# Kernel optimization log

Measured on AMD Instinct MI355X. Metric: run time of the kernel, lower is better.

The kernel has to match this reference:

```python
import jax, jax.numpy as jnp
import numpy as np

B, C, H, W = 4, 256, 48, 48
NH = 4                 # num_heads
HD = C // NH           # head_dim = 64
KD = HD // 2           # key_dim = 32 (attn_ratio=0.5)
QKV_C = C + 2 * KD * NH  # 512
FF = 2 * C             # 512
EPS = 1e-3             # ultralytics BatchNorm2d eps


def _bn(x, g, b, m, v):
    # eval-mode BatchNorm2d over channel dim 1 of NCHW
    s = g / jnp.sqrt(v + EPS)
    return x * s[:, None, None] + (b - m * s)[:, None, None]


def _conv1x1(x, w):
    # w: [out_c, in_c]
    return jnp.einsum('bchw,oc->bohw', x, w)


def _dwconv3x3(x, w):
    # depthwise 3x3, padding 1; w: [C, 1, 3, 3]
    return jax.lax.conv_general_dilated(
        x, w, (1, 1), [(1, 1), (1, 1)],
        dimension_numbers=('NCHW', 'OIHW', 'NCHW'),
        feature_group_count=C)


def setup_inputs() -> dict:
    key = jax.random.key(0)
    ks = jax.random.split(key, 32)
    d = {}
    d['x'] = jax.random.normal(ks[0], (B, C, H, W), dtype=jnp.float32)

    def bn_params(i, ch):
        g = 0.5 + jax.random.uniform(ks[i], (ch,), dtype=jnp.float32)
        b = 0.1 * jax.random.normal(ks[i + 1], (ch,), dtype=jnp.float32)
        m = 0.1 * jax.random.normal(ks[i + 2], (ch,), dtype=jnp.float32)
        v = 0.5 + jax.random.uniform(ks[i + 3], (ch,), dtype=jnp.float32)
        return g, b, m, v

    d['qkv_w'] = 0.05 * jax.random.normal(ks[1], (QKV_C, C), dtype=jnp.float32)
    d['qkv_g'], d['qkv_b'], d['qkv_m'], d['qkv_v'] = bn_params(2, QKV_C)
    d['pe_w'] = 0.1 * jax.random.normal(ks[6], (C, 1, 3, 3), dtype=jnp.float32)
    d['pe_g'], d['pe_b'], d['pe_m'], d['pe_v'] = bn_params(7, C)
    d['proj_w'] = 0.05 * jax.random.normal(ks[11], (C, C), dtype=jnp.float32)
    d['proj_g'], d['proj_b'], d['proj_m'], d['proj_v'] = bn_params(12, C)
    d['f1_w'] = 0.05 * jax.random.normal(ks[16], (FF, C), dtype=jnp.float32)
    d['f1_g'], d['f1_b'], d['f1_m'], d['f1_v'] = bn_params(17, FF)
    d['f2_w'] = 0.05 * jax.random.normal(ks[21], (C, FF), dtype=jnp.float32)
    d['f2_g'], d['f2_b'], d['f2_m'], d['f2_v'] = bn_params(22, C)
    return d


def reference(x, qkv_w, qkv_g, qkv_b, qkv_m, qkv_v,
              pe_w, pe_g, pe_b, pe_m, pe_v,
              proj_w, proj_g, proj_b, proj_m, proj_v,
              f1_w, f1_g, f1_b, f1_m, f1_v,
              f2_w, f2_g, f2_b, f2_m, f2_v):
    b, c, h, w = x.shape
    n = h * w
    # --- Attention ---
    qkv = _bn(_conv1x1(x, qkv_w), qkv_g, qkv_b, qkv_m, qkv_v)
    qkv = qkv.reshape(b, NH, 2 * KD + HD, n)
    q = qkv[:, :, :KD]            # [b, nh, kd, n]
    k = qkv[:, :, KD:2 * KD]      # [b, nh, kd, n]
    v = qkv[:, :, 2 * KD:]        # [b, nh, hd, n]
    attn = jnp.einsum('bhkn,bhkm->bhnm', q, k) * (KD ** -0.5)
    attn = jax.nn.softmax(attn, axis=-1)
    o = jnp.einsum('bhdm,bhnm->bhdn', v, attn).reshape(b, c, h, w)
    pe = _bn(_dwconv3x3(v.reshape(b, c, h, w), pe_w), pe_g, pe_b, pe_m, pe_v)
    attn_out = _bn(_conv1x1(o + pe, proj_w), proj_g, proj_b, proj_m, proj_v)
    x = x + attn_out  # shortcut
    # --- FFN ---
    f = _conv1x1(x, f1_w)
    f = _bn(f, f1_g, f1_b, f1_m, f1_v)
    f = f * jax.nn.sigmoid(f)  # SiLU
    f = _bn(_conv1x1(f, f2_w), f2_g, f2_b, f2_m, f2_v)
    return x + f  # shortcut
```

## Files before the change

kernel.cpp:

```cpp
#include <hip/hip_runtime.h>
#include <math.h>

#define Bb   4
#define Cc   256
#define Hh   48
#define Ww   48
#define NNp  2304
#define Rr   9216
#define NHd  4
#define QKVC 512
#define EPSf 1e-3f

typedef unsigned int   u32;
typedef unsigned short u16;
typedef __attribute__((ext_vector_type(8))) __bf16 bf16x8;
typedef __attribute__((ext_vector_type(4))) float  f32x4;

#if __has_builtin(__builtin_amdgcn_exp2f)
#define EXP2F(x) __builtin_amdgcn_exp2f(x)
#else
#define EXP2F(x) __expf((x) * 0.6931471805599453f)
#endif

__device__ __forceinline__ u16 f2bf(float f) {
    u32 u = __float_as_uint(f);
    u = (u + 0x7fffu + ((u >> 16) & 1u)) >> 16;
    return (u16)u;
}
__device__ __forceinline__ float bf2f(u16 h) {
    return __uint_as_float((u32)h << 16);
}
__device__ __forceinline__ u32 pk2bf(float a, float b) {
    union { __bf16 h; u16 u; } ua, ub;
    ua.h = (__bf16)a; ub.h = (__bf16)b;
    return (u32)ua.u | ((u32)ub.u << 16);
}
__device__ __forceinline__ void gload16(const void* gsrc, void* ldst) {
    __builtin_amdgcn_global_load_lds(
        (const __attribute__((address_space(1))) u32*)gsrc,
        (__attribute__((address_space(3))) u32*)ldst, 16, 0, 0);
}

__global__ __launch_bounds__(256)
void prep_fused(const float* __restrict__ W0, const float* __restrict__ g0, const float* __restrict__ b0, const float* __restrict__ m0, const float* __restrict__ v0, u16* __restrict__ Wb0, float* __restrict__ bi0,
                const float* __restrict__ W1, const float* __restrict__ g1, const float* __restrict__ b1, const float* __restrict__ m1, const float* __restrict__ v1, u16* __restrict__ Wb1, float* __restrict__ bi1,
                const float* __restrict__ W2, const float* __restrict__ g2, const float* __restrict__ b2, const float* __restrict__ m2, const float* __restrict__ v2, u16* __restrict__ Wb2, float* __restrict__ bi2,
                const float* __restrict__ W3, const float* __restrict__ g3, const float* __restrict__ b3, const float* __restrict__ m3, const float* __restrict__ v3, u16* __restrict__ Wb3, float* __restrict__ bi3,
                const float* __restrict__ x, u16* __restrict__ Xt)
{
    const int bid = blockIdx.x;
    const int tid = threadIdx.x;
    if (bid < 384) {
        const int row = bid * 4 + (tid >> 6);
        const int lane = tid & 63;
        const float *W, *gp, *bp, *mp, *vp;
        u16* Wb; float* bias;
        int K = 256, oc;
        float c = 1.f;
        if (row < 512) {
            oc = row; W = W0; gp = g0; bp = b0; mp = m0; vp = v0; Wb = Wb0; bias = bi0;
            if ((oc & 127) < 32) c = 0.17677669529663687f * 1.4426950408889634f;
        } else if (row < 768) {
            oc = row - 512; W = W1; gp = g1; bp = b1; mp = m1; vp = v1; Wb = Wb1; bias = bi1;
        } else if (row < 1280) {
            oc = row - 768; W = W2; gp = g2; bp = b2; mp = m2; vp = v2; Wb = Wb2; bias = bi2;
        } else {
            oc = row - 1280; W = W3; gp = g3; bp = b3; mp = m3; vp = v3; Wb = Wb3; bias = bi3;
            K = 512;
        }
        const float s = gp[oc] * rsqrtf(vp[oc] + EPSf);
        if (lane == 0) bias[oc] = (bp[oc] - mp[oc] * s) * c;
        const float sc = s * c;
        for (int k0 = lane * 4; k0 < K; k0 += 256) {
            const float4 w = *(const float4*)(W + (size_t)oc * K + k0);
            u32 lo = (u32)f2bf(w.x * sc) | ((u32)f2bf(w.y * sc) << 16);
            u32 hi = (u32)f2bf(w.z * sc) | ((u32)f2bf(w.w * sc) << 16);
            *(uint2*)(Wb + (size_t)oc * K + k0) = make_uint2(lo, hi);
        }
        return;
    }
    const int cb = bid - 384;
    const int b  = cb / 144;
    const int rm = cb - b * 144;
    const int c0 = (rm / 36) * 64;
    const int n0 = (rm % 36) * 64;
    __shared__ float tile[64][65];
    {
        const int n = tid & 63, cl = tid >> 6;
        #pragma unroll
        for (int cc = 0; cc < 16; ++cc) {
            const int c = cc * 4 + cl;
            tile[c][n] = x[((size_t)b * Cc + c0 + c) * NNp + n0 + n];
        }
    }
    __syncthreads();
    {
        const int n = tid >> 2, q = tid & 3;
        #pragma unroll
        for (int j = 0; j < 2; ++j) {
            const int ch = q * 2 + j, c = ch * 8;
            u32 w[4];
            #pragma unroll
            for (int e = 0; e < 4; ++e)
                w[e] = (u32)f2bf(tile[c + 2*e][n]) | ((u32)f2bf(tile[c + 2*e + 1][n]) << 16);
            *(uint4*)(Xt + ((size_t)b * NNp + n0 + n) * Cc + c0 + c)
                = make_uint4(w[0], w[1], w[2], w[3]);
        }
    }
}

template<int MODE>
__global__ __launch_bounds__(256)
void gemm64(const u16* __restrict__ A, const u16* __restrict__ Bx,
            const float* __restrict__ bias, const float* __restrict__ resid,
            float* __restrict__ Yf, u16* __restrict__ Yt, u16* __restrict__ Vb,
            int M, int K)
{
    const int r0 = blockIdx.x * 64;
    const int m0 = blockIdx.y * 64;
    const int tid = threadIdx.x;
    const int lane = tid & 63, wid = tid >> 6;
    const int g = lane >> 4, i16 = lane & 15;

    __shared__ __align__(16) u16 smem[2][2][4][64][8];

    f32x4 acc[4];
    #pragma unroll
    for (int j = 0; j < 4; ++j) acc[j] = (f32x4){0.f, 0.f, 0.f, 0.f};

    gload16(A + (size_t)(m0 + (tid & 63)) * K + (tid >> 6) * 8,
            &smem[0][0][0][0][0] + (size_t)tid * 8);
    gload16(Bx + (size_t)(r0 + (tid & 63)) * K + (tid >> 6) * 8,
            &smem[1][0][0][0][0] + (size_t)tid * 8);
    __syncthreads();

    int buf = 0;
    for (int k0 = 0; k0 < K; k0 += 32) {
        if (k0 + 32 < K) {
            const int kn = k0 + 32;
            gload16(A + (size_t)(m0 + (tid & 63)) * K + kn + (tid >> 6) * 8,
                    &smem[0][buf ^ 1][0][0][0] + (size_t)tid * 8);
            gload16(Bx + (size_t)(r0 + (tid & 63)) * K + kn + (tid >> 6) * 8,
                    &smem[1][buf ^ 1][0][0][0] + (size_t)tid * 8);
        }
        const bf16x8 af = *(const bf16x8*)&smem[0][buf][g][wid * 16 + i16][0];
        bf16x8 bf[4];
        #pragma unroll
        for (int bo = 0; bo < 4; ++bo)
            bf[bo] = *(const bf16x8*)&smem[1][buf][g][bo * 16 + i16][0];
        __builtin_amdgcn_s_setprio(1);
        #pragma unroll
        for (int bo = 0; bo < 4; ++bo)
            acc[bo] = __builtin_amdgcn_mfma_f32_16x16x32_bf16(af, bf[bo], acc[bo], 0, 0, 0);
        __builtin_amdgcn_s_setprio(0);
        __syncthreads();
        buf ^= 1;
    }

    const int b  = r0 / NNp;
    const int nb = r0 - b * NNp;
    const int oc0 = m0 + wid * 16 + g * 4;
    const float4 t4 = *(const float4*)(bias + oc0);
    const bool vblk = (MODE == 0) && (m0 & 64);
    u16 (*vt)[72] = (u16(*)[72])&smem[0][0][0][0][0];

    #pragma unroll
    for (int bo = 0; bo < 4; ++bo) {
        const int nloc = bo * 16 + i16;
        float y[4];
        y[0] = acc[bo][0] + t4.x;  y[1] = acc[bo][1] + t4.y;
        y[2] = acc[bo][2] + t4.z;  y[3] = acc[bo][3] + t4.w;
        if (MODE == 1 || MODE == 3) {
            const int n = nb + nloc;
            const size_t base = ((size_t)b * M + oc0) * NNp + n;
            #pragma unroll
            for (int r = 0; r < 4; ++r) {
                y[r] += resid[base + (size_t)r * NNp];
                Yf[base + (size_t)r * NNp] = y[r];
            }
        }
        if (MODE == 2) {
            #pragma unroll
            for (int r = 0; r < 4; ++r) y[r] = y[r] / (1.f + __expf(-y[r]));
        }
        if (MODE != 3) {
            const uint2 pk = make_uint2(pk2bf(y[0], y[1]), pk2bf(y[2], y[3]));
            *(uint2*)(Yt + (size_t)(r0 + nloc) * M + oc0) = pk;
            if (vblk) *(uint2*)&vt[nloc][wid * 16 + g * 4] = pk;
        }
    }

    if (vblk) {
        __syncthreads();
        const int h  = m0 >> 7;
        const int bh = b * NHd + h;
        const int d  = tid >> 2, mq = tid & 3;
        #pragma unroll
        for (int j = 0; j < 2; ++j) {
            const int mc = mq * 2 + j;
            u32 w[4];
            #pragma unroll
            for (int e = 0; e < 4; ++e)
                w[e] = (u32)vt[mc * 8 + 2*e][d] | ((u32)vt[mc * 8 + 2*e + 1][d] << 16);
            *(uint4*)(Vb + ((size_t)bh * 64 + d) * NNp + nb + mc * 8)
                = make_uint4(w[0], w[1], w[2], w[3]);
        }
    }
}

__global__ __launch_bounds__(256)
void pe_pre(const u16* __restrict__ Yt, const float* __restrict__ pw,
            const float* __restrict__ gg, const float* __restrict__ bb,
            const float* __restrict__ mm, const float* __restrict__ vv,
            u16* __restrict__ PEb)
{
    const int tid = threadIdx.x;
    const int h = blockIdx.y, b = blockIdx.z;
    const int p = blockIdx.x * 32 + (tid >> 3);
    const int ch = tid & 7;
    const int c0 = h * 64 + ch * 8;
    const int yy = p / Ww, xx = p - yy * Ww;

    float acc[8];
    #pragma unroll
    for (int j = 0; j < 8; ++j) acc[j] = 0.f;

    #pragma unroll
    for (int dy = -1; dy <= 1; ++dy) {
        const int Y = yy + dy;
        if (Y < 0 || Y >= Hh) continue;
        #pragma unroll
        for (int dx = -1; dx <= 1; ++dx) {
            const int X = xx + dx;
            if (X < 0 || X >= Ww) continue;
            const uint4 raw = *(const uint4*)(Yt +
                ((size_t)b * NNp + Y * Ww + X) * QKVC + h * 128 + 64 + ch * 8);
            const u32* rw = (const u32*)&raw;
            #pragma unroll
            for (int j = 0; j < 8; ++j) {
                const u16 hv = (u16)(rw[j >> 1] >> (16 * (j & 1)));
                acc[j] += pw[(size_t)(c0 + j) * 9 + (dy + 1) * 3 + (dx + 1)] * bf2f(hv);
            }
        }
    }

    u32 res[4];
    #pragma unroll
    for (int e = 0; e < 4; ++e) {
        const int j0 = 2 * e, j1 = 2 * e + 1;
        const float s0 = gg[c0 + j0] * rsqrtf(vv[c0 + j0] + EPSf);
        const float s1 = gg[c0 + j1] * rsqrtf(vv[c0 + j1] + EPSf);
        res[e] = pk2bf(acc[j0] * s0 + (bb[c0 + j0] - mm[c0 + j0] * s0),
                       acc[j1] * s1 + (bb[c0 + j1] - mm[c0 + j1] * s1));
    }
    *(uint4*)(PEb + ((size_t)b * NNp + p) * Cc + c0) = make_uint4(res[0], res[1], res[2], res[3]);
}

__global__ __launch_bounds__(128)
void attn_mfma(const u16* __restrict__ Yt, const u16* __restrict__ Vb,
               const u16* __restrict__ PEb, u16* __restrict__ Ot)
{
    __shared__ __align__(16) u16 Klds[2][4][64][8];
    __shared__ __align__(16) u16 Vlds[2][64][8][8];
    __shared__ __align__(16) u32 Plds[2][16][36];

    const int tid  = threadIdx.x;
    const int wid  = tid >> 6;
    const int lane = tid & 63;
    const int g    = lane >> 4;
    const int i16  = lane & 15;

    const int wg  = blockIdx.x;
    const int swz = (wg & 7) * 144 + (wg >> 3);
    const int xq  = swz % 72;
    const int bh  = swz / 72;
    const int h   = bh & 3, b = bh >> 2;

    const size_t bG = (size_t)b * NNp;
    const u16* Vg = Vb + (size_t)bh * 64 * NNp;

    const int nq = xq * 32 + wid * 16 + i16;
    const bf16x8 qfrag = *(const bf16x8*)(Yt + (bG + nq) * QKVC + h * 128 + g * 8);

    bf16x8 ones;
    { uint4 ov = make_uint4(0x3f803f80u, 0x3f803f80u, 0x3f803f80u, 0x3f803f80u);
      ones = *(bf16x8*)&ov; }

    const f32x4 zero = {0.f, 0.f, 0.f, 0.f};
    f32x4 oacc[4];
    f32x4 lacc = zero;
    #pragma unroll
    for (int d = 0; d < 4; ++d) oacc[d] = zero;
    float m_run = -1e30f;

    #pragma unroll
    for (int ii = 0; ii < 2; ++ii) {
        const int ci = ii * 128 + tid;
        gload16(Yt + (bG + (ci & 63)) * QKVC + h * 128 + 32 + (ci >> 6) * 8,
                (u16*)&Klds[0][0][0][0] + (size_t)ci * 8);
    }
    #pragma unroll
    for (int ii = 0; ii < 4; ++ii) {
        const int idx = ii * 128 + tid;
        const int d = idx >> 3, cp = idx & 7;
        gload16(Vg + (size_t)d * NNp + (cp ^ (d & 7)) * 8,
                (u16*)&Vlds[0][0][0][0] + (size_t)idx * 8);
    }
    __syncthreads();

    int cur = 0;
    for (int t = 0; t < 36; ++t) {
        if (t < 35) {
            const int m0 = (t + 1) * 64;
            #pragma unroll
            for (int ii = 0; ii < 2; ++ii) {
                const int ci = ii * 128 + tid;
                gload16(Yt + (bG + m0 + (ci & 63)) * QKVC + h * 128 + 32 + (ci >> 6) * 8,
                        (u16*)&Klds[cur ^ 1][0][0][0] + (size_t)ci * 8);
            }
            #pragma unroll
            for (int ii = 0; ii < 4; ++ii) {
                const int idx = ii * 128 + tid;
                const int d = idx >> 3, cp = idx & 7;
                gload16(Vg + (size_t)d * NNp + m0 + (cp ^ (d & 7)) * 8,
                        (u16*)&Vlds[cur ^ 1][0][0][0] + (size_t)idx * 8);
            }
        }

        f32x4 sac[4];
        __builtin_amdgcn_s_setprio(1);
        #pragma unroll
        for (int j = 0; j < 4; ++j) {
            const bf16x8 kf = *(const bf16x8*)&Klds[cur][g][16 * j + i16][0];
            sac[j] = __builtin_amdgcn_mfma_f32_16x16x32_bf16(kf, qfrag, zero, 0, 0, 0);
        }
        __builtin_amdgcn_s_setprio(0);

        float pm = sac[0][0];
        #pragma unroll
        for (int j = 0; j < 4; ++j)
            #pragma unroll
            for (int r = 0; r < 4; ++r) pm = fmaxf(pm, sac[j][r]);
        pm = fmaxf(pm, __shfl_xor(pm, 16));
        pm = fmaxf(pm, __shfl_xor(pm, 32));

        if (!__all(pm <= m_run + 8.f)) {
            const float mn = fmaxf(m_run, pm);
            const float fc = EXP2F(m_run - mn);
            m_run = mn;
            lacc[0] *= fc; lacc[1] *= fc; lacc[2] *= fc; lacc[3] *= fc;
            #pragma unroll
            for (int d = 0; d < 4; ++d) {
                oacc[d][0] *= fc; oacc[d][1] *= fc;
                oacc[d][2] *= fc; oacc[d][3] *= fc;
            }
        }

        {
            u32* prow = &Plds[wid][i16][0];
            #pragma unroll
            for (int j = 0; j < 4; ++j) {
                const float p0 = EXP2F(sac[j][0] - m_run);
                const float p1 = EXP2F(sac[j][1] - m_run);
                const float p2 = EXP2F(sac[j][2] - m_run);
                const float p3 = EXP2F(sac[j][3] - m_run);
                *(uint2*)&prow[8 * j + 2 * g] = make_uint2(pk2bf(p0, p1), pk2bf(p2, p3));
            }
        }

        const int d7 = i16 & 7;
        __builtin_amdgcn_s_setprio(1);
        #pragma unroll
        for (int s = 0; s < 2; ++s) {
            const bf16x8 pf = *(const bf16x8*)&Plds[wid][i16][16 * s + 4 * g];
            lacc = __builtin_amdgcn_mfma_f32_16x16x32_bf16(ones, pf, lacc, 0, 0, 0);
            #pragma unroll
            for (int db = 0; db < 4; ++db) {
                const bf16x8 vf = *(const bf16x8*)&Vlds[cur][db * 16 + i16][(4 * s + g) ^ d7][0];
                oacc[db] = __builtin_amdgcn_mfma_f32_16x16x32_bf16(vf, pf, oacc[db], 0, 0, 0);
            }
        }
        __builtin_amdgcn_s_setprio(0);

        __syncthreads();
        cur ^= 1;
    }

    const float linv = 1.f / lacc[0];
    const u16* pb = PEb + (bG + nq) * Cc + h * 64;
    u16* ob = Ot + (bG + nq) * Cc + h * 64;
    #pragma unroll
    for (int db = 0; db < 4; ++db) {
        const uint2 pv = *(const uint2*)(pb + db * 16 + g * 4);
        const float y0 = oacc[db][0] * linv + bf2f((u16)(pv.x & 0xffff));
        const float y1 = oacc[db][1] * linv + bf2f((u16)(pv.x >> 16));
        const float y2 = oacc[db][2] * linv + bf2f((u16)(pv.y & 0xffff));
        const float y3 = oacc[db][3] * linv + bf2f((u16)(pv.y >> 16));
        *(uint2*)(ob + db * 16 + g * 4) = make_uint2(pk2bf(y0, y1), pk2bf(y2, y3));
    }
}

extern "C" void kernel_launch(void* const* d_in, const int* in_sizes, int n_in,
                              void* d_out, int out_size, void* d_ws, size_t ws_size,
                              hipStream_t stream)
{
    const float* x      = (const float*)d_in[0];
    const float* qkv_w  = (const float*)d_in[1];
    const float* qkv_g  = (const float*)d_in[2];
    const float* qkv_b  = (const float*)d_in[3];
    const float* qkv_m  = (const float*)d_in[4];
    const float* qkv_v  = (const float*)d_in[5];
    const float* pe_w   = (const float*)d_in[6];
    const float* pe_g   = (const float*)d_in[7];
    const float* pe_b   = (const float*)d_in[8];
    const float* pe_m   = (const float*)d_in[9];
    const float* pe_v   = (const float*)d_in[10];
    const float* proj_w = (const float*)d_in[11];
    const float* proj_g = (const float*)d_in[12];
    const float* proj_b = (const float*)d_in[13];
    const float* proj_m = (const float*)d_in[14];
    const float* proj_v = (const float*)d_in[15];
    const float* f1_w   = (const float*)d_in[16];
    const float* f1_g   = (const float*)d_in[17];
    const float* f1_b   = (const float*)d_in[18];
    const float* f1_m   = (const float*)d_in[19];
    const float* f1_v   = (const float*)d_in[20];
    const float* f2_w   = (const float*)d_in[21];
    const float* f2_g   = (const float*)d_in[22];
    const float* f2_b   = (const float*)d_in[23];
    const float* f2_m   = (const float*)d_in[24];
    const float* f2_v   = (const float*)d_in[25];

    char* wsb = (char*)d_ws;
    u16*   Yt   = (u16*)(wsb);
    u16*   Xt   = (u16*)(wsb + 9437184);
    u16*   Vb   = (u16*)(wsb + 14155776);
    u16*   Ot   = (u16*)(wsb + 18874368);
    float* x1f  = (float*)(wsb + 23592960);
    u16*   PEb  = (u16*)(wsb + 23592960);
    u16*   Wq   = (u16*)(wsb + 33030144);
    u16*   Wp   = (u16*)(wsb + 33292288);
    u16*   W1   = (u16*)(wsb + 33423360);
    u16*   W2   = (u16*)(wsb + 33685504);
    float* biq  = (float*)(wsb + 33947648);
    float* bip  = (float*)(wsb + 33949696);
    float* bi1  = (float*)(wsb + 33950720);
    float* bi2  = (float*)(wsb + 33952768);
    u16*   Ft   = Yt;
    u16*   X1t  = Xt;
    float* out  = (float*)d_out;

    prep_fused<<<dim3(960), dim3(256), 0, stream>>>(
        qkv_w, qkv_g, qkv_b, qkv_m, qkv_v, Wq, biq,
        proj_w, proj_g, proj_b, proj_m, proj_v, Wp, bip,
        f1_w, f1_g, f1_b, f1_m, f1_v, W1, bi1,
        f2_w, f2_g, f2_b, f2_m, f2_v, W2, bi2,
        x, Xt);

    gemm64<0><<<dim3(144, 8), dim3(256), 0, stream>>>(
        Wq, Xt, biq, nullptr, nullptr, Yt, Vb, QKVC, 256);

    pe_pre<<<dim3(72, 4, 4), dim3(256), 0, stream>>>(
        Yt, pe_w, pe_g, pe_b, pe_m, pe_v, PEb);

    attn_mfma<<<dim3(1152), dim3(128), 0, stream>>>(Yt, Vb, PEb, Ot);

    gemm64<1><<<dim3(144, 4), dim3(256), 0, stream>>>(
        Wp, Ot, bip, x, x1f, X1t, nullptr, Cc, 256);

    gemm64<2><<<dim3(144, 8), dim3(256), 0, stream>>>(
        W1, X1t, bi1, nullptr, nullptr, Ft, nullptr, QKVC, 256);

    gemm64<3><<<dim3(144, 4), dim3(256), 0, stream>>>(
        W2, Ft, bi2, x1f, out, nullptr, nullptr, Cc, 512);
}
```

Baseline: 141.6 us.

## Triple-buffer attention K/V tiles with 32-key steps and single barrier

Replaces the double-buffered 64-key tile loop with a 3-stage ring of 32-key tiles. Each iteration does a partial vmcnt wait and one barrier before it issues the prefetch two tiles ahead, and the trailing __syncthreads is removed. V is stored in LDS in an MFMA-fragment layout instead of the XOR swizzle, and P/LDS footprints shrink. The aim is to hide global-load latency and cut LDS use. In exchange it doubles the iteration count and the per-tile max/rescale checks, and the correctness of the buffer reuse depends on the waitcnt accounting.

```diff
diff --git a/kernel.cpp b/kernel.cpp
--- a/kernel.cpp
+++ b/kernel.cpp
@@ -260,9 +260,9 @@
 void attn_mfma(const u16* __restrict__ Yt, const u16* __restrict__ Vb,
                const u16* __restrict__ PEb, u16* __restrict__ Ot)
 {
-    __shared__ __align__(16) u16 Klds[2][4][64][8];
-    __shared__ __align__(16) u16 Vlds[2][64][8][8];
-    __shared__ __align__(16) u32 Plds[2][16][36];
+    __shared__ __align__(16) u16 Klds[3][4][32][8];
+    __shared__ __align__(16) u16 Vlds[3][4][4][16][8];
+    __shared__ __align__(16) u32 Plds[2][16][20];
 
     const int tid  = threadIdx.x;
     const int wid  = tid >> 6;
@@ -293,54 +293,52 @@
     for (int d = 0; d < 4; ++d) oacc[d] = zero;
     float m_run = -1e30f;
 
-    #pragma unroll
-    for (int ii = 0; ii < 2; ++ii) {
-        const int ci = ii * 128 + tid;
-        gload16(Yt + (bG + (ci & 63)) * QKVC + h * 128 + 32 + (ci >> 6) * 8,
-                (u16*)&Klds[0][0][0][0] + (size_t)ci * 8);
-    }
-    #pragma unroll
-    for (int ii = 0; ii < 4; ++ii) {
-        const int idx = ii * 128 + tid;
-        const int d = idx >> 3, cp = idx & 7;
-        gload16(Vg + (size_t)d * NNp + (cp ^ (d & 7)) * 8,
-                (u16*)&Vlds[0][0][0][0] + (size_t)idx * 8);
-    }
-    __syncthreads();
+    const int krow = tid & 31, kch = tid >> 5;
+    const int vd0  = ((tid >> 6) << 4) + (tid & 15);
+    const int vc0  = (tid >> 4) & 3;
+    const int vd1  = (((128 + tid) >> 6) << 4) + (tid & 15);
+    const int vc1  = ((128 + tid) >> 4) & 3;
+
+    #pragma unroll
+    for (int tt = 0; tt < 2; ++tt) {
+        gload16(Yt + (bG + tt * 32 + krow) * QKVC + h * 128 + 32 + kch * 8,
+                (u16*)&Klds[tt][0][0][0] + (size_t)tid * 8);
+        gload16(Vg + (size_t)vd0 * NNp + tt * 32 + vc0 * 8,
+                (u16*)&Vlds[tt][0][0][0][0] + (size_t)tid * 8);
+        gload16(Vg + (size_t)vd1 * NNp + tt * 32 + vc1 * 8,
+                (u16*)&Vlds[tt][0][0][0][0] + (size_t)(128 + tid) * 8);
+    }
 
     int cur = 0;
-    for (int t = 0; t < 36; ++t) {
-        if (t < 35) {
-            const int m0 = (t + 1) * 64;
-            #pragma unroll
-            for (int ii = 0; ii < 2; ++ii) {
-                const int ci = ii * 128 + tid;
-                gload16(Yt + (bG + m0 + (ci & 63)) * QKVC + h * 128 + 32 + (ci >> 6) * 8,
-                        (u16*)&Klds[cur ^ 1][0][0][0] + (size_t)ci * 8);
-            }
-            #pragma unroll
-            for (int ii = 0; ii < 4; ++ii) {
-                const int idx = ii * 128 + tid;
-                const int d = idx >> 3, cp = idx & 7;
-                gload16(Vg + (size_t)d * NNp + m0 + (cp ^ (d & 7)) * 8,
-                        (u16*)&Vlds[cur ^ 1][0][0][0] + (size_t)idx * 8);
-            }
-        }
-
-        f32x4 sac[4];
+    for (int t = 0; t < 72; ++t) {
+        asm volatile("s_waitcnt vmcnt(3)" ::: "memory");
+        __builtin_amdgcn_sched_barrier(0);
+        __builtin_amdgcn_s_barrier();
+        __builtin_amdgcn_sched_barrier(0);
+
+        if (t + 2 < 72) {
+            const int mn = (t + 2) * 32;
+            const int bn = (cur + 2 >= 3) ? cur - 1 : cur + 2;
+            gload16(Yt + (bG + mn + krow) * QKVC + h * 128 + 32 + kch * 8,
+                    (u16*)&Klds[bn][0][0][0] + (size_t)tid * 8);
+            gload16(Vg + (size_t)vd0 * NNp + mn + vc0 * 8,
+                    (u16*)&Vlds[bn][0][0][0][0] + (size_t)tid * 8);
+            gload16(Vg + (size_t)vd1 * NNp + mn + vc1 * 8,
+                    (u16*)&Vlds[bn][0][0][0][0] + (size_t)(128 + tid) * 8);
+        }
+
+        f32x4 sac[2];
         __builtin_amdgcn_s_setprio(1);
         #pragma unroll
-        for (int j = 0; j < 4; ++j) {
+        for (int j = 0; j < 2; ++j) {
             const bf16x8 kf = *(const bf16x8*)&Klds[cur][g][16 * j + i16][0];
             sac[j] = __builtin_amdgcn_mfma_f32_16x16x32_bf16(kf, qfrag, zero, 0, 0, 0);
         }
         __builtin_amdgcn_s_setprio(0);
 
-        float pm = sac[0][0];
-        #pragma unroll
-        for (int j = 0; j < 4; ++j)
-            #pragma unroll
-            for (int r = 0; r < 4; ++r) pm = fmaxf(pm, sac[j][r]);
+        float pm = fmaxf(fmaxf(fmaxf(sac[0][0], sac[0][1]), sac[0][2]),
+                         fmaxf(fmaxf(sac[0][3], sac[1][0]),
+                               fmaxf(sac[1][1], fmaxf(sac[1][2], sac[1][3]))));
         pm = fmaxf(pm, __shfl_xor(pm, 16));
         pm = fmaxf(pm, __shfl_xor(pm, 32));
 
@@ -359,7 +357,7 @@
         {
             u32* prow = &Plds[wid][i16][0];
             #pragma unroll
-            for (int j = 0; j < 4; ++j) {
+            for (int j = 0; j < 2; ++j) {
                 const float p0 = EXP2F(sac[j][0] - m_run);
                 const float p1 = EXP2F(sac[j][1] - m_run);
                 const float p2 = EXP2F(sac[j][2] - m_run);
@@ -368,22 +366,19 @@
             }
         }
 
-        const int d7 = i16 & 7;
         __builtin_amdgcn_s_setprio(1);
-        #pragma unroll
-        for (int s = 0; s < 2; ++s) {
-            const bf16x8 pf = *(const bf16x8*)&Plds[wid][i16][16 * s + 4 * g];
+        {
+            const bf16x8 pf = *(const bf16x8*)&Plds[wid][i16][4 * g];
             lacc = __builtin_amdgcn_mfma_f32_16x16x32_bf16(ones, pf, lacc, 0, 0, 0);
             #pragma unroll
             for (int db = 0; db < 4; ++db) {
-                const bf16x8 vf = *(const bf16x8*)&Vlds[cur][db * 16 + i16][(4 * s + g) ^ d7][0];
+                const bf16x8 vf = *(const bf16x8*)&Vlds[cur][db][g][i16][0];
                 oacc[db] = __builtin_amdgcn_mfma_f32_16x16x32_bf16(vf, pf, oacc[db], 0, 0, 0);
             }
         }
         __builtin_amdgcn_s_setprio(0);
 
-        __syncthreads();
-        cur ^= 1;
+        cur = (cur == 2) ? 0 : cur + 1;
     }
 
     const float linv = 1.f / lacc[0];
```

Result: slower. 157.4 us (+11.1%).

## Switch attention to 32x32x16 MFMA with register-resident P via permlane32 swap

Applied to the files above, without the earlier changes.

Rewrites the attention kernel to use 32x32x16 bf16 MFMA tiles, giving each wave 32 queries, so the grid is halved and K/V tiles loaded into LDS are reused across twice as many queries. The P matrix is no longer round-tripped through LDS; it is rearranged in registers with permlane32_swap to form the B operand of the PV MFMA. The row sum is computed with VALU adds instead of an MFMA against a ones vector. This cuts LDS traffic and MFMA instruction count, at the cost of more accumulator registers per wave and fewer workgroups, which can lower occupancy.

```diff
diff --git a/kernel.cpp b/kernel.cpp
--- a/kernel.cpp
+++ b/kernel.cpp
@@ -13,8 +13,9 @@
 
 typedef unsigned int   u32;
 typedef unsigned short u16;
-typedef __attribute__((ext_vector_type(8))) __bf16 bf16x8;
-typedef __attribute__((ext_vector_type(4))) float  f32x4;
+typedef __attribute__((ext_vector_type(8)))  __bf16 bf16x8;
+typedef __attribute__((ext_vector_type(4)))  float  f32x4;
+typedef __attribute__((ext_vector_type(16))) float  f32x16;
 
 #if __has_builtin(__builtin_amdgcn_exp2f)
 #define EXP2F(x) __builtin_amdgcn_exp2f(x)
@@ -262,36 +263,33 @@
 {
     __shared__ __align__(16) u16 Klds[2][4][64][8];
     __shared__ __align__(16) u16 Vlds[2][64][8][8];
-    __shared__ __align__(16) u32 Plds[2][16][36];
 
     const int tid  = threadIdx.x;
     const int wid  = tid >> 6;
     const int lane = tid & 63;
-    const int g    = lane >> 4;
-    const int i16  = lane & 15;
+    const int hi   = lane >> 5;
+    const int kl   = lane & 31;
 
     const int wg  = blockIdx.x;
-    const int swz = (wg & 7) * 144 + (wg >> 3);
-    const int xq  = swz % 72;
-    const int bh  = swz / 72;
+    const int swz = (wg & 7) * 72 + (wg >> 3);
+    const int xq  = swz % 36;
+    const int bh  = swz / 36;
     const int h   = bh & 3, b = bh >> 2;
 
     const size_t bG = (size_t)b * NNp;
     const u16* Vg = Vb + (size_t)bh * 64 * NNp;
 
-    const int nq = xq * 32 + wid * 16 + i16;
-    const bf16x8 qfrag = *(const bf16x8*)(Yt + (bG + nq) * QKVC + h * 128 + g * 8);
-
-    bf16x8 ones;
-    { uint4 ov = make_uint4(0x3f803f80u, 0x3f803f80u, 0x3f803f80u, 0x3f803f80u);
-      ones = *(bf16x8*)&ov; }
-
-    const f32x4 zero = {0.f, 0.f, 0.f, 0.f};
-    f32x4 oacc[4];
-    f32x4 lacc = zero;
-    #pragma unroll
-    for (int d = 0; d < 4; ++d) oacc[d] = zero;
-    float m_run = -1e30f;
+    const int nq = xq * 64 + wid * 32 + kl;
+    bf16x8 qf[2];
+    qf[0] = *(const bf16x8*)(Yt + (bG + nq) * QKVC + h * 128 + 8 * hi);
+    qf[1] = *(const bf16x8*)(Yt + (bG + nq) * QKVC + h * 128 + 16 + 8 * hi);
+
+    f32x16 z16;
+    #pragma unroll
+    for (int i = 0; i < 16; ++i) z16[i] = 0.f;
+    f32x16 oacc[2];
+    oacc[0] = z16; oacc[1] = z16;
+    float m_run = -1e30f, l_run = 0.f;
 
     #pragma unroll
     for (int ii = 0; ii < 2; ++ii) {
@@ -327,57 +325,70 @@
             }
         }
 
-        f32x4 sac[4];
+        f32x16 sac[2];
         __builtin_amdgcn_s_setprio(1);
         #pragma unroll
-        for (int j = 0; j < 4; ++j) {
-            const bf16x8 kf = *(const bf16x8*)&Klds[cur][g][16 * j + i16][0];
-            sac[j] = __builtin_amdgcn_mfma_f32_16x16x32_bf16(kf, qfrag, zero, 0, 0, 0);
+        for (int kb = 0; kb < 2; ++kb) {
+            const bf16x8 kf0 = *(const bf16x8*)&Klds[cur][hi][32 * kb + kl][0];
+            const bf16x8 kf1 = *(const bf16x8*)&Klds[cur][2 + hi][32 * kb + kl][0];
+            sac[kb] = __builtin_amdgcn_mfma_f32_32x32x16_bf16(kf0, qf[0], z16, 0, 0, 0);
+            sac[kb] = __builtin_amdgcn_mfma_f32_32x32x16_bf16(kf1, qf[1], sac[kb], 0, 0, 0);
         }
         __builtin_amdgcn_s_setprio(0);
 
         float pm = sac[0][0];
         #pragma unroll
-        for (int j = 0; j < 4; ++j)
-            #pragma unroll
-            for (int r = 0; r < 4; ++r) pm = fmaxf(pm, sac[j][r]);
-        pm = fmaxf(pm, __shfl_xor(pm, 16));
+        for (int r = 1; r < 16; ++r) pm = fmaxf(pm, sac[0][r]);
+        #pragma unroll
+        for (int r = 0; r < 16; ++r) pm = fmaxf(pm, sac[1][r]);
         pm = fmaxf(pm, __shfl_xor(pm, 32));
 
         if (!__all(pm <= m_run + 8.f)) {
             const float mn = fmaxf(m_run, pm);
             const float fc = EXP2F(m_run - mn);
             m_run = mn;
-            lacc[0] *= fc; lacc[1] *= fc; lacc[2] *= fc; lacc[3] *= fc;
-            #pragma unroll
-            for (int d = 0; d < 4; ++d) {
-                oacc[d][0] *= fc; oacc[d][1] *= fc;
-                oacc[d][2] *= fc; oacc[d][3] *= fc;
-            }
-        }
-
-        {
-            u32* prow = &Plds[wid][i16][0];
-            #pragma unroll
-            for (int j = 0; j < 4; ++j) {
-                const float p0 = EXP2F(sac[j][0] - m_run);
-                const float p1 = EXP2F(sac[j][1] - m_run);
-                const float p2 = EXP2F(sac[j][2] - m_run);
-                const float p3 = EXP2F(sac[j][3] - m_run);
-                *(uint2*)&prow[8 * j + 2 * g] = make_uint2(pk2bf(p0, p1), pk2bf(p2, p3));
-            }
-        }
-
-        const int d7 = i16 & 7;
+            l_run *= fc;
+            #pragma unroll
+            for (int kb = 0; kb < 2; ++kb)
+                #pragma unroll
+                for (int i = 0; i < 16; ++i) oacc[kb][i] *= fc;
+        }
+
+        float psum = 0.f;
+        u32 w[2][4][2];
+        #pragma unroll
+        for (int kb = 0; kb < 2; ++kb)
+            #pragma unroll
+            for (int u = 0; u < 4; ++u)
+                #pragma unroll
+                for (int v = 0; v < 2; ++v) {
+                    const float a  = EXP2F(sac[kb][4 * u + 2 * v]     - m_run);
+                    const float b2 = EXP2F(sac[kb][4 * u + 2 * v + 1] - m_run);
+                    psum += a + b2;
+                    w[kb][u][v] = pk2bf(a, b2);
+                }
+        psum += __shfl_xor(psum, 32);
+        l_run += psum;
+
+        const int c7 = kl & 7;
         __builtin_amdgcn_s_setprio(1);
         #pragma unroll
-        for (int s = 0; s < 2; ++s) {
-            const bf16x8 pf = *(const bf16x8*)&Plds[wid][i16][16 * s + 4 * g];
-            lacc = __builtin_amdgcn_mfma_f32_16x16x32_bf16(ones, pf, lacc, 0, 0, 0);
-            #pragma unroll
-            for (int db = 0; db < 4; ++db) {
-                const bf16x8 vf = *(const bf16x8*)&Vlds[cur][db * 16 + i16][(4 * s + g) ^ d7][0];
-                oacc[db] = __builtin_amdgcn_mfma_f32_16x16x32_bf16(vf, pf, oacc[db], 0, 0, 0);
+        for (int kb = 0; kb < 2; ++kb) {
+            #pragma unroll
+            for (int m = 0; m < 2; ++m) {
+                auto r0 = __builtin_amdgcn_permlane32_swap(
+                    w[kb][2 * m][0], w[kb][2 * m + 1][0], false, false);
+                auto r1 = __builtin_amdgcn_permlane32_swap(
+                    w[kb][2 * m][1], w[kb][2 * m + 1][1], false, false);
+                const uint4 fw = make_uint4(r0[0], r1[0], r0[1], r1[1]);
+                const bf16x8 pf = *(const bf16x8*)&fw;
+                const int ch = (4 * kb + 2 * m + hi) ^ c7;
+                #pragma unroll
+                for (int dblk = 0; dblk < 2; ++dblk) {
+                    const bf16x8 vf = *(const bf16x8*)&Vlds[cur][dblk * 32 + kl][ch][0];
+                    oacc[dblk] = __builtin_amdgcn_mfma_f32_32x32x16_bf16(
+                        vf, pf, oacc[dblk], 0, 0, 0);
+                }
             }
         }
         __builtin_amdgcn_s_setprio(0);
@@ -386,18 +397,21 @@
         cur ^= 1;
     }
 
-    const float linv = 1.f / lacc[0];
+    const float linv = 1.f / l_run;
     const u16* pb = PEb + (bG + nq) * Cc + h * 64;
     u16* ob = Ot + (bG + nq) * Cc + h * 64;
     #pragma unroll
-    for (int db = 0; db < 4; ++db) {
-        const uint2 pv = *(const uint2*)(pb + db * 16 + g * 4);
-        const float y0 = oacc[db][0] * linv + bf2f((u16)(pv.x & 0xffff));
-        const float y1 = oacc[db][1] * linv + bf2f((u16)(pv.x >> 16));
-        const float y2 = oacc[db][2] * linv + bf2f((u16)(pv.y & 0xffff));
-        const float y3 = oacc[db][3] * linv + bf2f((u16)(pv.y >> 16));
-        *(uint2*)(ob + db * 16 + g * 4) = make_uint2(pk2bf(y0, y1), pk2bf(y2, y3));
-    }
+    for (int dblk = 0; dblk < 2; ++dblk)
+        #pragma unroll
+        for (int rg = 0; rg < 4; ++rg) {
+            const int d0 = dblk * 32 + rg * 8 + 4 * hi;
+            const uint2 pv = *(const uint2*)(pb + d0);
+            const float y0 = oacc[dblk][4 * rg + 0] * linv + bf2f((u16)(pv.x & 0xffff));
+            const float y1 = oacc[dblk][4 * rg + 1] * linv + bf2f((u16)(pv.x >> 16));
+            const float y2 = oacc[dblk][4 * rg + 2] * linv + bf2f((u16)(pv.y & 0xffff));
+            const float y3 = oacc[dblk][4 * rg + 3] * linv + bf2f((u16)(pv.y >> 16));
+            *(uint2*)(ob + d0) = make_uint2(pk2bf(y0, y1), pk2bf(y2, y3));
+        }
 }
 
 extern "C" void kernel_launch(void* const* d_in, const int* in_sizes, int n_in,
@@ -463,7 +477,7 @@
     pe_pre<<<dim3(72, 4, 4), dim3(256), 0, stream>>>(
         Yt, pe_w, pe_g, pe_b, pe_m, pe_v, PEb);
 
-    attn_mfma<<<dim3(1152), dim3(128), 0, stream>>>(Yt, Vb, PEb, Ot);
+    attn_mfma<<<dim3(576), dim3(128), 0, stream>>>(Yt, Vb, PEb, Ot);
 
     gemm64<1><<<dim3(144, 4), dim3(256), 0, stream>>>(
         Wp, Ot, bip, x, x1f, X1t, nullptr, Cc, 256);
```

After: 158.9 us. 1.12x slower.
